# Kernel optimization log

Measured on AMD Instinct MI355X. Metric: run time of the kernel, lower is better.

## Reference

```python
import jax, jax.numpy as jnp
import numpy as np

B, S, D = 2, 2048, 1024
H, HD = 16, 64          # num_heads, head_dim = D // H
C = 8                   # subspace_dim of the equivariant relative-position basis
EPS = 1e-6              # flax LayerNorm default epsilon


def setup_inputs() -> dict:
    key = jax.random.key(0)
    ks = jax.random.split(key, 12)
    sd = 0.02
    return {
        "x": jax.random.normal(ks[0], (B, S, D), jnp.float32),
        "Q_basis": jax.random.normal(ks[1], (S, S, C), jnp.float32),
        "Wq": jax.random.normal(ks[2], (D, H, HD), jnp.float32) * sd,
        "bq": jnp.zeros((H, HD), jnp.float32),
        "Wk": jax.random.normal(ks[3], (D, H, HD), jnp.float32) * sd,
        "bk": jnp.zeros((H, HD), jnp.float32),
        "Wv": jax.random.normal(ks[4], (D, H, HD), jnp.float32) * sd,
        "bv": jnp.zeros((H, HD), jnp.float32),
        "q_ln_scale": jnp.ones((HD,), jnp.float32),
        "k_ln_scale": jnp.ones((HD,), jnp.float32),
        "relative_attn": jax.random.normal(ks[5], (C, H), jnp.float32) * sd,
        "Wo": jax.random.normal(ks[6], (H, HD, D), jnp.float32) * sd,
        "bo": jnp.zeros((D,), jnp.float32),
    }


def _layernorm(x, scale):
    # LayerNorm over last axis, use_bias=False
    mu = jnp.mean(x, axis=-1, keepdims=True)
    var = jnp.mean(jnp.square(x - mu), axis=-1, keepdims=True)
    return (x - mu) * jax.lax.rsqrt(var + EPS) * scale


def reference(x, Q_basis, Wq, bq, Wk, bk, Wv, bv,
              q_ln_scale, k_ln_scale, relative_attn, Wo, bo):
    # QKV projections: [B,S,D] x [D,H,HD] -> [B,S,H,HD]
    q = jnp.einsum('bsd,dhk->bshk', x, Wq) + bq
    k = jnp.einsum('bsd,dhk->bshk', x, Wk) + bk
    v = jnp.einsum('bsd,dhk->bshk', x, Wv) + bv
    # QK layernorm over head_dim
    q = _layernorm(q, q_ln_scale)
    k = _layernorm(k, k_ln_scale)
    # Learned relative-position bias: [C,H] x [S,S,C] -> [H,S,S]
    bias = jnp.einsum('ch,qkc->hqk', relative_attn, Q_basis)
    # Scaled dot-product attention with bias (matches nn.dot_product_attention)
    scores = jnp.einsum('bqhd,bkhd->bhqk', q, k) / jnp.sqrt(jnp.float32(HD))
    attn = jax.nn.softmax(scores + bias, axis=-1)
    ctx = jnp.einsum('bhqk,bkhd->bqhd', attn, v)
    # Output projection over (heads, head_dim) -> D
    return jnp.einsum('bqhd,hdo->bqo', ctx, Wo) + bo
```

## Files before the change

kernel.cpp:

```cpp
#include <hip/hip_runtime.h>

typedef float f32x4 __attribute__((ext_vector_type(4)));
typedef __bf16 bf16x8 __attribute__((ext_vector_type(8)));
typedef unsigned short u16x8 __attribute__((ext_vector_type(8)));
typedef unsigned short u16x4 __attribute__((ext_vector_type(4)));

#define AS1 __attribute__((address_space(1)))
#define AS3 __attribute__((address_space(3)))

static __device__ __forceinline__ void gll16(const void* g, void* l) {
  __builtin_amdgcn_global_load_lds((const AS1 void*)g, (AS3 void*)l, 16, 0, 0);
}

static __device__ __forceinline__ float bf2f(unsigned short u) {
  unsigned int x = ((unsigned int)u) << 16;
  float f; __builtin_memcpy(&f, &x, 4); return f;
}
static __device__ __forceinline__ unsigned short f2bf(float f) {
  unsigned int x; __builtin_memcpy(&x, &f, 4);
  unsigned int r = (x + 0x7fffu + ((x >> 16) & 1u)) >> 16;
  return (unsigned short)r;
}

#define LOG2E 1.4426950408889634f
#define QSCALE (0.125f * LOG2E)

__global__ __launch_bounds__(256) void k_cvt_x(const float* __restrict__ x,
                                               unsigned short* __restrict__ xb) {
  int i = (blockIdx.x * 256 + threadIdx.x) * 4;
  float4 v = *(const float4*)(x + i);
  u16x4 o; o.x = f2bf(v.x); o.y = f2bf(v.y); o.z = f2bf(v.z); o.w = f2bf(v.w);
  *(u16x4*)(xb + i) = o;
}

__global__ __launch_bounds__(256) void k_transpose(const float* __restrict__ w0,
                                                   const float* __restrict__ w1,
                                                   const float* __restrict__ w2,
                                                   const float* __restrict__ w3,
                                                   unsigned short* __restrict__ dqkv,
                                                   unsigned short* __restrict__ dwo) {
  __shared__ float tile[32][33];
  int z = blockIdx.z;
  const float* src = (z == 0) ? w0 : (z == 1) ? w1 : (z == 2) ? w2 : w3;
  unsigned short* dst = (z < 3) ? (dqkv + (size_t)z * 1024 * 1024) : dwo;
  int tx = threadIdx.x, ty = threadIdx.y;
  int x0 = blockIdx.x * 32, y0 = blockIdx.y * 32;
#pragma unroll
  for (int i = 0; i < 4; ++i)
    tile[ty + 8 * i][tx] = src[(size_t)(y0 + ty + 8 * i) * 1024 + x0 + tx];
  __syncthreads();
#pragma unroll
  for (int i = 0; i < 4; ++i)
    dst[(size_t)(x0 + ty + 8 * i) * 1024 + y0 + tx] = f2bf(tile[tx][ty + 8 * i]);
}

__global__ __launch_bounds__(256) void k_bias(const float* __restrict__ Qb,
                                              const float* __restrict__ R,
                                              unsigned short* __restrict__ bias) {
  __shared__ float Rs[8][16];
  int t = threadIdx.x;
  if (t < 128) Rs[t >> 4][t & 15] = R[t] * LOG2E;
  __syncthreads();
  int q = blockIdx.x;
  int k = t * 8;
  const float* src = Qb + ((size_t)q * 2048 + k) * 8;
  float a[8][8];
#pragma unroll
  for (int kk = 0; kk < 8; ++kk) {
    float4 lo = *(const float4*)(src + kk * 8);
    float4 hi = *(const float4*)(src + kk * 8 + 4);
    a[kk][0] = lo.x; a[kk][1] = lo.y; a[kk][2] = lo.z; a[kk][3] = lo.w;
    a[kk][4] = hi.x; a[kk][5] = hi.y; a[kk][6] = hi.z; a[kk][7] = hi.w;
  }
#pragma unroll
  for (int h = 0; h < 16; ++h) {
    u16x8 o;
#pragma unroll
    for (int kk = 0; kk < 8; ++kk) {
      float s = 0.f;
#pragma unroll
      for (int c = 0; c < 8; ++c) s += a[kk][c] * Rs[c][h];
      o[kk] = f2bf(s);
    }
    *(u16x8*)(bias + ((size_t)h * 2048 + q) * 2048 + k) = o;
  }
}

__global__ __launch_bounds__(256) void k_qkv(const unsigned short* __restrict__ xb,
                                             const unsigned short* __restrict__ wt,
                                             const float* __restrict__ bq,
                                             const float* __restrict__ bk,
                                             const float* __restrict__ bv,
                                             const float* __restrict__ qls,
                                             const float* __restrict__ kls,
                                             unsigned short* __restrict__ qo,
                                             unsigned short* __restrict__ kqo,
                                             unsigned short* __restrict__ vo) {
  __shared__ unsigned short As[4096];
  __shared__ unsigned short Bs[4096];
  const int tid = threadIdx.x;
  const int w = tid >> 6, lane = tid & 63, quad = lane >> 4, lx = lane & 15;
  const int m0 = blockIdx.y * 128, n0 = blockIdx.x * 128;
  const int wrow = w >> 1, wcol = w & 1;

  f32x4 acc[4][4];
#pragma unroll
  for (int i = 0; i < 4; ++i)
#pragma unroll
    for (int j = 0; j < 4; ++j) acc[i][j] = (f32x4){0.f, 0.f, 0.f, 0.f};

  const unsigned short* ga = xb + (size_t)(m0 + 32 * w + (lane >> 2)) * 1024 + (lane & 3) * 8;
  const unsigned short* gb = wt + (size_t)(n0 + 32 * w + (lane >> 2)) * 1024 + (lane & 3) * 8;
  unsigned short* la = As + w * 1024;
  unsigned short* lb = Bs + w * 1024;

  for (int kt = 0; kt < 32; ++kt) {
    const int kofs = kt * 32;
    gll16(ga + kofs, la);
    gll16(ga + kofs + 16 * 1024, la + 512);
    gll16(gb + kofs, lb);
    gll16(gb + kofs + 16 * 1024, lb + 512);
    __syncthreads();
    bf16x8 af[4], bfr[4];
#pragma unroll
    for (int i = 0; i < 4; ++i)
      af[i] = *(const bf16x8*)&As[(64 * wrow + 16 * i + lx) * 32 + quad * 8];
#pragma unroll
    for (int j = 0; j < 4; ++j)
      bfr[j] = *(const bf16x8*)&Bs[(64 * wcol + 16 * j + lx) * 32 + quad * 8];
#pragma unroll
    for (int i = 0; i < 4; ++i)
#pragma unroll
      for (int j = 0; j < 4; ++j)
        acc[i][j] = __builtin_amdgcn_mfma_f32_16x16x32_bf16(af[i], bfr[j], acc[i][j], 0, 0, 0);
    __syncthreads();
  }

  const int colbase = n0 + 64 * wcol;
  const int region = colbase >> 10;
  const int h = (colbase & 1023) >> 6;
  const float* pbp = (region == 0) ? bq : (region == 1) ? bk : bv;
  float pb[4];
#pragma unroll
  for (int j = 0; j < 4; ++j) pb[j] = pbp[h * 64 + j * 16 + lx];

  if (region == 2) {
#pragma unroll
    for (int i = 0; i < 4; ++i) {
#pragma unroll
      for (int rr = 0; rr < 4; ++rr) {
        int m = m0 + 64 * wrow + 16 * i + quad * 4 + rr;
        int b = m >> 11, s = m & 2047;
        unsigned short* dst = vo + ((size_t)b * 16 + h) * 64 * 2048 + s;
#pragma unroll
        for (int j = 0; j < 4; ++j)
          dst[(size_t)(j * 16 + lx) * 2048] = f2bf(acc[i][j][rr] + pb[j]);
      }
    }
  } else {
    const float fac = region ? 1.0f : QSCALE;
    float scl[4];
    const float* lsp = region ? kls : qls;
#pragma unroll
    for (int j = 0; j < 4; ++j) scl[j] = lsp[j * 16 + lx] * fac;
    unsigned short* base = region ? kqo : qo;
#pragma unroll
    for (int i = 0; i < 4; ++i) {
#pragma unroll
      for (int rr = 0; rr < 4; ++rr) {
        int m = m0 + 64 * wrow + 16 * i + quad * 4 + rr;
        int b = m >> 11, s = m & 2047;
        float v0 = acc[i][0][rr] + pb[0];
        float v1 = acc[i][1][rr] + pb[1];
        float v2 = acc[i][2][rr] + pb[2];
        float v3 = acc[i][3][rr] + pb[3];
        float s1 = v0 + v1 + v2 + v3;
        float s2 = v0 * v0 + v1 * v1 + v2 * v2 + v3 * v3;
#pragma unroll
        for (int d = 1; d < 16; d <<= 1) {
          s1 += __shfl_xor(s1, d, 64);
          s2 += __shfl_xor(s2, d, 64);
        }
        float mu = s1 * 0.015625f;
        float var = s2 * 0.015625f - mu * mu;
        float ri = __builtin_amdgcn_rsqf(var + 1e-6f);
        unsigned short* dst = base + (((size_t)b * 16 + h) * 2048 + s) * 64;
        dst[0 * 16 + lx] = f2bf((v0 - mu) * ri * scl[0]);
        dst[1 * 16 + lx] = f2bf((v1 - mu) * ri * scl[1]);
        dst[2 * 16 + lx] = f2bf((v2 - mu) * ri * scl[2]);
        dst[3 * 16 + lx] = f2bf((v3 - mu) * ri * scl[3]);
      }
    }
  }
}

__global__ __launch_bounds__(256) void k_attn(const unsigned short* __restrict__ qp,
                                              const unsigned short* __restrict__ kp,
                                              const unsigned short* __restrict__ vp,
                                              const unsigned short* __restrict__ bp,
                                              unsigned short* __restrict__ ctx) {
  __shared__ unsigned short Ks[8192];
  __shared__ unsigned short Vs[8192];
  __shared__ unsigned short Ps[9216];
  const int tid = threadIdx.x;
  const int w = tid >> 6, lane = tid & 63, quad = lane >> 4, lx = lane & 15;
  const int bb = w >> 1, ww = w & 1;
  const int qt = blockIdx.x, h = blockIdx.y;
  const int q0 = qt * 64;
  const size_t bh = (size_t)bb * 16 + h;

  const unsigned short* qgp = qp + (bh * 2048 + q0 + ww * 32) * 64;
  bf16x8 qf[2][2];
#pragma unroll
  for (int qg = 0; qg < 2; ++qg)
#pragma unroll
    for (int hh = 0; hh < 2; ++hh)
      qf[qg][hh] = *(const bf16x8*)(qgp + (qg * 16 + lx) * 64 + hh * 32 + quad * 8);

  const int r8 = lane >> 3;
  const int cA = (lane & 7) ^ r8;
  const unsigned short* kgs = kp + bh * 2048 * 64 + (ww * 32 + r8) * 64 + cA * 8;
  const unsigned short* vgs = vp + bh * 64 * 2048 + (size_t)(ww * 32 + r8) * 2048 + cA * 8;
  unsigned short* ldk = Ks + bb * 4096 + ww * 2048;
  unsigned short* ldv = Vs + bb * 4096 + ww * 2048;
  const unsigned short* bg = bp + ((size_t)h * 2048 + q0 + ww * 32) * 2048;
  unsigned short* psw = Ps + w * 2304;

  float l_run[2] = {0.f, 0.f};
  f32x4 acco[2][4];
#pragma unroll
  for (int qg = 0; qg < 2; ++qg)
#pragma unroll
    for (int j = 0; j < 4; ++j) acco[qg][j] = (f32x4){0.f, 0.f, 0.f, 0.f};

  for (int kt = 0; kt < 32; ++kt) {
    const int k0 = kt * 64;
#pragma unroll
    for (int idx = 0; idx < 4; ++idx) {
      gll16(kgs + (size_t)(k0 + idx * 8) * 64, ldk + idx * 512);
      gll16(vgs + k0 + idx * 8 * 2048, ldv + idx * 512);
    }
    uint2 bu[2][4];
#pragma unroll
    for (int qg = 0; qg < 2; ++qg)
#pragma unroll
      for (int j = 0; j < 4; ++j)
        bu[qg][j] = *(const uint2*)(bg + (size_t)(qg * 16 + lx) * 2048 + k0 + j * 16 + quad * 4);
    __syncthreads();

    bf16x8 kf[4][2];
#pragma unroll
    for (int j = 0; j < 4; ++j)
#pragma unroll
      for (int hh = 0; hh < 2; ++hh)
        kf[j][hh] = *(const bf16x8*)&Ks[bb * 4096 + (j * 16 + lx) * 64 +
                                        (((hh * 4 + quad) ^ (lx & 7)) * 8)];
#pragma unroll
    for (int qg = 0; qg < 2; ++qg) {
      f32x4 accs[4];
#pragma unroll
      for (int j = 0; j < 4; ++j) {
        accs[j][0] = __uint_as_float(bu[qg][j].x << 16);
        accs[j][1] = __uint_as_float(bu[qg][j].x & 0xffff0000u);
        accs[j][2] = __uint_as_float(bu[qg][j].y << 16);
        accs[j][3] = __uint_as_float(bu[qg][j].y & 0xffff0000u);
      }
#pragma unroll
      for (int hh = 0; hh < 2; ++hh)
#pragma unroll
        for (int j = 0; j < 4; ++j)
          accs[j] = __builtin_amdgcn_mfma_f32_16x16x32_bf16(kf[j][hh], qf[qg][hh], accs[j], 0, 0, 0);
#pragma unroll
      for (int j = 0; j < 4; ++j) {
        float p0 = __builtin_amdgcn_exp2f(accs[j][0]);
        float p1 = __builtin_amdgcn_exp2f(accs[j][1]);
        float p2 = __builtin_amdgcn_exp2f(accs[j][2]);
        float p3 = __builtin_amdgcn_exp2f(accs[j][3]);
        l_run[qg] += (p0 + p1) + (p2 + p3);
        unsigned int a0 = __float_as_uint(p0) + 0x8000u;
        unsigned int a1 = __float_as_uint(p1) + 0x8000u;
        unsigned int a2 = __float_as_uint(p2) + 0x8000u;
        unsigned int a3 = __float_as_uint(p3) + 0x8000u;
        uint2 pk;
        pk.x = __builtin_amdgcn_perm(a1, a0, 0x07060302u);
        pk.y = __builtin_amdgcn_perm(a3, a2, 0x07060302u);
        *(uint2*)&psw[(qg * 16 + lx) * 72 + j * 16 + quad * 4] = pk;
      }
    }
    __asm__ volatile("s_waitcnt lgkmcnt(0)" ::: "memory");
    bf16x8 vf[4][2];
#pragma unroll
    for (int j = 0; j < 4; ++j)
#pragma unroll
      for (int kh = 0; kh < 2; ++kh)
        vf[j][kh] = *(const bf16x8*)&Vs[bb * 4096 + (j * 16 + lx) * 64 +
                                        (((kh * 4 + quad) ^ (lx & 7)) * 8)];
#pragma unroll
    for (int qg = 0; qg < 2; ++qg) {
      bf16x8 pf[2];
#pragma unroll
      for (int kh = 0; kh < 2; ++kh)
        pf[kh] = *(const bf16x8*)&psw[(qg * 16 + lx) * 72 + kh * 32 + quad * 8];
#pragma unroll
      for (int kh = 0; kh < 2; ++kh)
#pragma unroll
        for (int j = 0; j < 4; ++j)
          acco[qg][j] = __builtin_amdgcn_mfma_f32_16x16x32_bf16(pf[kh], vf[j][kh], acco[qg][j], 0, 0, 0);
    }
    __syncthreads();
  }

#pragma unroll
  for (int qg = 0; qg < 2; ++qg) {
    float l = l_run[qg];
    l += __shfl_xor(l, 16, 64);
    l += __shfl_xor(l, 32, 64);
#pragma unroll
    for (int rr = 0; rr < 4; ++rr) {
      float lq = __shfl(l, quad * 4 + rr, 64);
      float rl = __builtin_amdgcn_rcpf(lq);
      int q = q0 + ww * 32 + qg * 16 + quad * 4 + rr;
      unsigned short* dst = ctx + (((size_t)bb * 2048 + q) * 16 + h) * 64;
#pragma unroll
      for (int j = 0; j < 4; ++j) dst[j * 16 + lx] = f2bf(acco[qg][j][rr] * rl);
    }
  }
}

__global__ __launch_bounds__(256) void k_out(const unsigned short* __restrict__ cx,
                                             const unsigned short* __restrict__ wt,
                                             const float* __restrict__ bo,
                                             float* __restrict__ out) {
  __shared__ unsigned short As[4096];
  __shared__ unsigned short Bs[4096];
  const int tid = threadIdx.x;
  const int w = tid >> 6, lane = tid & 63, quad = lane >> 4, lx = lane & 15;
  const int m0 = blockIdx.y * 128, n0 = blockIdx.x * 128;
  const int wrow = w >> 1, wcol = w & 1;

  f32x4 acc[4][4];
#pragma unroll
  for (int i = 0; i < 4; ++i)
#pragma unroll
    for (int j = 0; j < 4; ++j) acc[i][j] = (f32x4){0.f, 0.f, 0.f, 0.f};

  const unsigned short* ga = cx + (size_t)(m0 + 32 * w + (lane >> 2)) * 1024 + (lane & 3) * 8;
  const unsigned short* gb = wt + (size_t)(n0 + 32 * w + (lane >> 2)) * 1024 + (lane & 3) * 8;
  unsigned short* la = As + w * 1024;
  unsigned short* lb = Bs + w * 1024;

  for (int kt = 0; kt < 32; ++kt) {
    const int kofs = kt * 32;
    gll16(ga + kofs, la);
    gll16(ga + kofs + 16 * 1024, la + 512);
    gll16(gb + kofs, lb);
    gll16(gb + kofs + 16 * 1024, lb + 512);
    __syncthreads();
    bf16x8 af[4], bfr[4];
#pragma unroll
    for (int i = 0; i < 4; ++i)
      af[i] = *(const bf16x8*)&As[(64 * wrow + 16 * i + lx) * 32 + quad * 8];
#pragma unroll
    for (int j = 0; j < 4; ++j)
      bfr[j] = *(const bf16x8*)&Bs[(64 * wcol + 16 * j + lx) * 32 + quad * 8];
#pragma unroll
    for (int i = 0; i < 4; ++i)
#pragma unroll
      for (int j = 0; j < 4; ++j)
        acc[i][j] = __builtin_amdgcn_mfma_f32_16x16x32_bf16(af[i], bfr[j], acc[i][j], 0, 0, 0);
    __syncthreads();
  }

  const int colbase = n0 + 64 * wcol;
  float bb[4];
#pragma unroll
  for (int j = 0; j < 4; ++j) bb[j] = bo[colbase + j * 16 + lx];
#pragma unroll
  for (int i = 0; i < 4; ++i) {
#pragma unroll
    for (int rr = 0; rr < 4; ++rr) {
      int m = m0 + 64 * wrow + 16 * i + quad * 4 + rr;
      float* dst = out + (size_t)m * 1024 + colbase;
#pragma unroll
      for (int j = 0; j < 4; ++j) dst[j * 16 + lx] = acc[i][j][rr] + bb[j];
    }
  }
}

extern "C" void kernel_launch(void* const* d_in, const int* in_sizes, int n_in,
                              void* d_out, int out_size, void* d_ws, size_t ws_size,
                              hipStream_t stream) {
  (void)in_sizes; (void)n_in; (void)out_size; (void)ws_size;
  const float* x   = (const float*)d_in[0];
  const float* Qb  = (const float*)d_in[1];
  const float* Wq  = (const float*)d_in[2];
  const float* bq  = (const float*)d_in[3];
  const float* Wk  = (const float*)d_in[4];
  const float* bk  = (const float*)d_in[5];
  const float* Wv  = (const float*)d_in[6];
  const float* bv  = (const float*)d_in[7];
  const float* qls = (const float*)d_in[8];
  const float* kls = (const float*)d_in[9];
  const float* Ra  = (const float*)d_in[10];
  const float* Wo  = (const float*)d_in[11];
  const float* bo  = (const float*)d_in[12];
  float* out = (float*)d_out;

  char* ws = (char*)d_ws;
  unsigned short* xb    = (unsigned short*)(ws + 0);
  unsigned short* wqkvt = (unsigned short*)(ws + 8388608);
  unsigned short* wot   = (unsigned short*)(ws + 14680064);
  unsigned short* qb    = (unsigned short*)(ws + 16777216);
  unsigned short* kb    = (unsigned short*)(ws + 25165824);
  unsigned short* vtb   = (unsigned short*)(ws + 33554432);
  unsigned short* ctxb  = (unsigned short*)(ws + 41943040);
  unsigned short* biasb = (unsigned short*)(ws + 50331648);

  k_cvt_x<<<4096, 256, 0, stream>>>(x, xb);
  k_transpose<<<dim3(32, 32, 4), dim3(32, 8), 0, stream>>>(Wq, Wk, Wv, Wo, wqkvt, wot);
  k_bias<<<2048, 256, 0, stream>>>(Qb, Ra, biasb);
  k_qkv<<<dim3(24, 32), 256, 0, stream>>>(xb, wqkvt, bq, bk, bv, qls, kls, qb, kb, vtb);
  k_attn<<<dim3(32, 16), 256, 0, stream>>>(qb, kb, vtb, biasb, ctxb);
  k_out<<<dim3(8, 32), 256, 0, stream>>>(ctxb, wot, bo, out);
}
```

Before: 461.8 us.

## Split attention key range across two wave groups and reduce partials in LDS

Doubles the attention block to 512 threads so that two wave groups each handle half of the key sequence for the same query tile, then combine their partial output accumulators and row sums through shared memory. The P tile buffer is made smaller and XOR-swizzled, and the V fragment loads are hoisted alongside the K loads. The goal is more waves in flight per block to hide latency. In exchange, LDS use per block grows to 80 KB and a final cross-group reduction is added. The unnormalized exp without a running max stays as before.

```diff
diff --git a/kernel.cpp b/kernel.cpp
--- a/kernel.cpp
+++ b/kernel.cpp
@@ -194,17 +194,21 @@
   }
 }
 
-__global__ __launch_bounds__(256) void k_attn(const unsigned short* __restrict__ qp,
-                                              const unsigned short* __restrict__ kp,
-                                              const unsigned short* __restrict__ vp,
-                                              const unsigned short* __restrict__ bp,
-                                              unsigned short* __restrict__ ctx) {
-  __shared__ unsigned short Ks[8192];
-  __shared__ unsigned short Vs[8192];
-  __shared__ unsigned short Ps[9216];
+__global__ __launch_bounds__(512, 4) void k_attn(const unsigned short* __restrict__ qp,
+                                                 const unsigned short* __restrict__ kp,
+                                                 const unsigned short* __restrict__ vp,
+                                                 const unsigned short* __restrict__ bp,
+                                                 unsigned short* __restrict__ ctx) {
+  __shared__ char smem[81920];
+  unsigned short* Ks = (unsigned short*)smem;
+  unsigned short* Vs = (unsigned short*)(smem + 32768);
+  unsigned short* Ps = (unsigned short*)(smem + 65536);
+
   const int tid = threadIdx.x;
   const int w = tid >> 6, lane = tid & 63, quad = lane >> 4, lx = lane & 15;
-  const int bb = w >> 1, ww = w & 1;
+  const int lx7 = lane & 7;
+  const int bb = w >> 2, kh = (w >> 1) & 1, ww = w & 1;
+  const int str = bb * 2 + kh;
   const int qt = blockIdx.x, h = blockIdx.y;
   const int q0 = qt * 64;
   const size_t bh = (size_t)bb * 16 + h;
@@ -218,13 +222,13 @@
       qf[qg][hh] = *(const bf16x8*)(qgp + (qg * 16 + lx) * 64 + hh * 32 + quad * 8);
 
   const int r8 = lane >> 3;
-  const int cA = (lane & 7) ^ r8;
+  const int cA = (lane & 7) ^ (r8 & 7);
   const unsigned short* kgs = kp + bh * 2048 * 64 + (ww * 32 + r8) * 64 + cA * 8;
   const unsigned short* vgs = vp + bh * 64 * 2048 + (size_t)(ww * 32 + r8) * 2048 + cA * 8;
-  unsigned short* ldk = Ks + bb * 4096 + ww * 2048;
-  unsigned short* ldv = Vs + bb * 4096 + ww * 2048;
+  unsigned short* ldk = Ks + str * 4096 + ww * 2048;
+  unsigned short* ldv = Vs + str * 4096 + ww * 2048;
   const unsigned short* bg = bp + ((size_t)h * 2048 + q0 + ww * 32) * 2048;
-  unsigned short* psw = Ps + w * 2304;
+  unsigned short* psw = Ps + w * 1024;
 
   float l_run[2] = {0.f, 0.f};
   f32x4 acco[2][4];
@@ -233,8 +237,8 @@
 #pragma unroll
     for (int j = 0; j < 4; ++j) acco[qg][j] = (f32x4){0.f, 0.f, 0.f, 0.f};
 
-  for (int kt = 0; kt < 32; ++kt) {
-    const int k0 = kt * 64;
+  for (int kt = 0; kt < 16; ++kt) {
+    const int k0 = kh * 1024 + kt * 64;
 #pragma unroll
     for (int idx = 0; idx < 4; ++idx) {
       gll16(kgs + (size_t)(k0 + idx * 8) * 64, ldk + idx * 512);
@@ -248,13 +252,16 @@
         bu[qg][j] = *(const uint2*)(bg + (size_t)(qg * 16 + lx) * 2048 + k0 + j * 16 + quad * 4);
     __syncthreads();
 
-    bf16x8 kf[4][2];
+    bf16x8 kf[4][2], vf[4][2];
 #pragma unroll
     for (int j = 0; j < 4; ++j)
 #pragma unroll
-      for (int hh = 0; hh < 2; ++hh)
-        kf[j][hh] = *(const bf16x8*)&Ks[bb * 4096 + (j * 16 + lx) * 64 +
-                                        (((hh * 4 + quad) ^ (lx & 7)) * 8)];
+      for (int hh = 0; hh < 2; ++hh) {
+        kf[j][hh] = *(const bf16x8*)&Ks[str * 4096 + (j * 16 + lx) * 64 +
+                                        (((hh * 4 + quad) ^ lx7) * 8)];
+        vf[j][hh] = *(const bf16x8*)&Vs[str * 4096 + (j * 16 + lx) * 64 +
+                                        (((hh * 4 + quad) ^ lx7) * 8)];
+      }
 #pragma unroll
     for (int qg = 0; qg < 2; ++qg) {
       f32x4 accs[4];
@@ -284,45 +291,56 @@
         uint2 pk;
         pk.x = __builtin_amdgcn_perm(a1, a0, 0x07060302u);
         pk.y = __builtin_amdgcn_perm(a3, a2, 0x07060302u);
-        *(uint2*)&psw[(qg * 16 + lx) * 72 + j * 16 + quad * 4] = pk;
-      }
-    }
-    __asm__ volatile("s_waitcnt lgkmcnt(0)" ::: "memory");
-    bf16x8 vf[4][2];
-#pragma unroll
-    for (int j = 0; j < 4; ++j)
-#pragma unroll
-      for (int kh = 0; kh < 2; ++kh)
-        vf[j][kh] = *(const bf16x8*)&Vs[bb * 4096 + (j * 16 + lx) * 64 +
-                                        (((kh * 4 + quad) ^ (lx & 7)) * 8)];
+        const int chunk = ((j * 2 + (quad >> 1)) ^ lx7);
+        *(uint2*)&psw[lx * 64 + chunk * 8 + (quad & 1) * 4] = pk;
+      }
+      __asm__ volatile("s_waitcnt lgkmcnt(0)" ::: "memory");
+      bf16x8 pf[2];
+#pragma unroll
+      for (int kh2 = 0; kh2 < 2; ++kh2)
+        pf[kh2] = *(const bf16x8*)&psw[lx * 64 + (((kh2 * 4 + quad) ^ lx7) * 8)];
+      __asm__ volatile("s_waitcnt lgkmcnt(0)" ::: "memory");
+#pragma unroll
+      for (int kh2 = 0; kh2 < 2; ++kh2)
+#pragma unroll
+        for (int j = 0; j < 4; ++j)
+          acco[qg][j] = __builtin_amdgcn_mfma_f32_16x16x32_bf16(pf[kh2], vf[j][kh2], acco[qg][j], 0, 0, 0);
+    }
+    __syncthreads();
+  }
+
+  float* os = (float*)(smem + (bb * 2 + ww) * 8704);
+  if (kh == 1) {
+#pragma unroll
+    for (int qg = 0; qg < 2; ++qg)
+#pragma unroll
+      for (int j = 0; j < 4; ++j)
+        *(f32x4*)(os + ((qg * 4 + j) * 64 + lane) * 4) = acco[qg][j];
+    *(float2*)(os + 2048 + lane * 2) = make_float2(l_run[0], l_run[1]);
+  }
+  __syncthreads();
+  if (kh == 0) {
+    float2 lp = *(const float2*)(os + 2048 + lane * 2);
+    l_run[0] += lp.x; l_run[1] += lp.y;
 #pragma unroll
     for (int qg = 0; qg < 2; ++qg) {
-      bf16x8 pf[2];
-#pragma unroll
-      for (int kh = 0; kh < 2; ++kh)
-        pf[kh] = *(const bf16x8*)&psw[(qg * 16 + lx) * 72 + kh * 32 + quad * 8];
-#pragma unroll
-      for (int kh = 0; kh < 2; ++kh)
-#pragma unroll
-        for (int j = 0; j < 4; ++j)
-          acco[qg][j] = __builtin_amdgcn_mfma_f32_16x16x32_bf16(pf[kh], vf[j][kh], acco[qg][j], 0, 0, 0);
-    }
-    __syncthreads();
-  }
-
-#pragma unroll
-  for (int qg = 0; qg < 2; ++qg) {
-    float l = l_run[qg];
-    l += __shfl_xor(l, 16, 64);
-    l += __shfl_xor(l, 32, 64);
-#pragma unroll
-    for (int rr = 0; rr < 4; ++rr) {
-      float lq = __shfl(l, quad * 4 + rr, 64);
-      float rl = __builtin_amdgcn_rcpf(lq);
-      int q = q0 + ww * 32 + qg * 16 + quad * 4 + rr;
-      unsigned short* dst = ctx + (((size_t)bb * 2048 + q) * 16 + h) * 64;
-#pragma unroll
-      for (int j = 0; j < 4; ++j) dst[j * 16 + lx] = f2bf(acco[qg][j][rr] * rl);
+#pragma unroll
+      for (int j = 0; j < 4; ++j) {
+        f32x4 o2 = *(const f32x4*)(os + ((qg * 4 + j) * 64 + lane) * 4);
+        acco[qg][j] += o2;
+      }
+      float l = l_run[qg];
+      l += __shfl_xor(l, 16, 64);
+      l += __shfl_xor(l, 32, 64);
+#pragma unroll
+      for (int rr = 0; rr < 4; ++rr) {
+        float lq = __shfl(l, quad * 4 + rr, 64);
+        float rl = __builtin_amdgcn_rcpf(lq);
+        int q = q0 + ww * 32 + qg * 16 + quad * 4 + rr;
+        unsigned short* dst = ctx + (((size_t)bb * 2048 + q) * 16 + h) * 64;
+#pragma unroll
+        for (int j = 0; j < 4; ++j) dst[j * 16 + lx] = f2bf(acco[qg][j][rr] * rl);
+      }
     }
   }
 }
@@ -420,6 +438,6 @@
   k_transpose<<<dim3(32, 32, 4), dim3(32, 8), 0, stream>>>(Wq, Wk, Wv, Wo, wqkvt, wot);
   k_bias<<<2048, 256, 0, stream>>>(Qb, Ra, biasb);
   k_qkv<<<dim3(24, 32), 256, 0, stream>>>(xb, wqkvt, bq, bk, bv, qls, kls, qb, kb, vtb);
-  k_attn<<<dim3(32, 16), 256, 0, stream>>>(qb, kb, vtb, biasb, ctxb);
+  k_attn<<<dim3(32, 16), 512, 0, stream>>>(qb, kb, vtb, biasb, ctxb);
   k_out<<<dim3(8, 32), 256, 0, stream>>>(ctxb, wot, bo, out);
 }
```

After: 510.7 us. 1.11x slower.
